# Kernel tuning notes

Measured on AMD Instinct MI355X. Metric: run time of the kernel, lower is better.

## Reference

```python
import jax, jax.numpy as jnp
import numpy as np

N_NODES = 20000
N_EDGES = 640000
IN_FEATS = 128
H1, H2 = 64, 32


def setup_inputs() -> dict:
    key = jax.random.key(0)
    ks = jax.random.split(key, 7)
    features = jax.random.normal(ks[0], (N_NODES, IN_FEATS), dtype=jnp.float32)
    W1 = jax.random.normal(ks[1], (IN_FEATS, H1), dtype=jnp.float32) * (1.0 / np.sqrt(IN_FEATS))
    b1 = jax.random.normal(ks[2], (H1,), dtype=jnp.float32) * 0.01
    W2 = jax.random.normal(ks[3], (H1, H2), dtype=jnp.float32) * (1.0 / np.sqrt(H1))
    b2 = jax.random.normal(ks[4], (H2,), dtype=jnp.float32) * 0.01
    src = jax.random.randint(ks[5], (N_EDGES,), 0, N_NODES, dtype=jnp.int32)
    dst = jax.random.randint(ks[6], (N_EDGES,), 0, N_NODES, dtype=jnp.int32)
    return {"features": features, "W1": W1, "b1": b1, "W2": W2, "b2": b2,
            "src": src, "dst": dst}


def _gcn_aggregate(h, src, dst, n_nodes):
    # copy_u + sum: gather source-node features along edges, sum at destinations
    return jax.ops.segment_sum(h[src], dst, num_segments=n_nodes)


def reference(features, W1, b1, W2, b2, src, dst):
    n = features.shape[0]
    # layer 1: aggregate then linear, relu
    h = _gcn_aggregate(features, src, dst, n)          # [N, in_feats]
    x = jax.nn.relu(h @ W1 + b1)                       # [N, 64]
    # layer 2: aggregate then linear
    h2 = _gcn_aggregate(x, src, dst, n)                # [N, 64]
    return h2 @ W2 + b2                                # [N, 32]
```

## Files before the change

### kernel.cpp

```cpp
#include <hip/hip_runtime.h>


#define NF 128
#define H1 64
#define H2 32
#define CAP 128
#define CAPSH 7
#define NG8 8
#define SCHUNK 1024
#define FILL_BPG 80

__device__ __forceinline__ float blo(unsigned u){ return __uint_as_float(u << 16); }
__device__ __forceinline__ float bhi(unsigned u){ return __uint_as_float(u & 0xffff0000u); }
__device__ __forceinline__ unsigned short f2b(float f){
    unsigned x = __float_as_uint(f);
    return (unsigned short)((x + 0x7fffu + ((x >> 16) & 1u)) >> 16);
}

__launch_bounds__(256)
__global__ void k1_kernel(const float* __restrict__ F, const float* __restrict__ W1,
                          const int* __restrict__ src, const int* __restrict__ dst,
                          unsigned* __restrict__ staged, int* __restrict__ bofs,
                          unsigned short* __restrict__ P1b, int* __restrict__ cnt,
                          unsigned inv_sz, int n_nodes, int n_edges, int nsb) {
    __shared__ __align__(16) float w[NF * H1];
    __shared__ int lcnt[NG8 + 1];
    const int t = threadIdx.x;
    const int bid = blockIdx.x;

    if (bid < nsb) {
        unsigned* sorted = (unsigned*)w;
        int e0 = bid * SCHUNK;
        int ce = min(n_edges - e0, SCHUNK);
        if (t < NG8 + 1) lcnt[t] = 0;
        __syncthreads();
        int i4 = e0 + t * 4;
        int dd[4], ss[4], bb[4], pp[4];
        if (i4 + 4 <= n_edges) {
            int4 d4 = *(const int4*)(dst + i4);
            int4 s4 = *(const int4*)(src + i4);
            dd[0]=d4.x; dd[1]=d4.y; dd[2]=d4.z; dd[3]=d4.w;
            ss[0]=s4.x; ss[1]=s4.y; ss[2]=s4.z; ss[3]=s4.w;
        } else {
#pragma unroll
            for (int k = 0; k < 4; ++k) {
                int e = i4 + k;
                dd[k] = (e < n_edges) ? dst[e] : -1;
                ss[k] = (e < n_edges) ? src[e] : 0;
            }
        }
#pragma unroll
        for (int k = 0; k < 4; ++k) {
            if (dd[k] >= 0) {
                bb[k] = (int)(unsigned)(((unsigned long long)(unsigned)dd[k] * inv_sz) >> 32);
                pp[k] = atomicAdd(&lcnt[bb[k]], 1);
            }
        }
        __syncthreads();
        if (t == 0) {
            int run = 0;
#pragma unroll
            for (int i = 0; i < NG8 + 1; ++i) { int c = lcnt[i]; lcnt[i] = run; run += c; }
        }
        __syncthreads();
#pragma unroll
        for (int k = 0; k < 4; ++k)
            if (dd[k] >= 0)
                sorted[lcnt[bb[k]] + pp[k]] = ((unsigned)dd[k] << 16) | (unsigned)ss[k];
        __syncthreads();
        for (int j = t; j < ce; j += 256) staged[(size_t)bid * SCHUNK + j] = sorted[j];
        if (t < NG8 + 1) bofs[t * nsb + bid] = lcnt[t];
        return;
    }

    int gb = bid - nsb;
    int zi = gb * 256 + t;
    if (zi < n_nodes) cnt[zi] = 0;
    {
        const float4* w4 = (const float4*)W1;
        float4* ws4 = (float4*)w;
#pragma unroll
        for (int j = 0; j < 8; ++j) ws4[t + 256 * j] = w4[t + 256 * j];
    }
    __syncthreads();
    int wid = t >> 6, lane = t & 63;
    int row0 = gb * 32 + wid * 8;
#pragma unroll
    for (int r = 0; r < 8; ++r) {
        int row = row0 + r;
        if (row >= n_nodes) break;
        const float4* f4 = (const float4*)(F + (size_t)row * NF);
        float acc = 0.f;
#pragma unroll 8
        for (int k4 = 0; k4 < NF / 4; ++k4) {
            float4 fv = f4[k4];
            acc += fv.x * w[(k4 * 4 + 0) * H1 + lane];
            acc += fv.y * w[(k4 * 4 + 1) * H1 + lane];
            acc += fv.z * w[(k4 * 4 + 2) * H1 + lane];
            acc += fv.w * w[(k4 * 4 + 3) * H1 + lane];
        }
        P1b[(size_t)row * H1 + lane] = f2b(acc);
    }
}

__launch_bounds__(256)
__global__ void fill2_kernel(const unsigned* __restrict__ staged, const int* __restrict__ bofs,
                             int* __restrict__ cnt, unsigned short* __restrict__ slots,
                             int nsb) {
    int g = blockIdx.x & (NG8 - 1), gi = blockIdx.x >> 3;
    for (int sb = gi; sb < nsb; sb += FILL_BPG) {
        int st = bofs[g * nsb + sb];
        int en = bofs[(g + 1) * nsb + sb];
        const unsigned* seg = staged + (size_t)sb * SCHUNK;
        for (int j = st + threadIdx.x; j < en; j += 256) {
            unsigned u = seg[j];
            int d = u >> 16;
            int p = atomicAdd(&cnt[d], 1);
            if (p < CAP) slots[(d << CAPSH) + p] = (unsigned short)(u & 0xffffu);
        }
    }
}

__launch_bounds__(256)
__global__ void agg1gemm2_kernel(const unsigned short* __restrict__ P1b,
                                 const int* __restrict__ cnt, const unsigned short* __restrict__ slots,
                                 const float* __restrict__ b1, const float* __restrict__ W2,
                                 unsigned short* __restrict__ P2b, int n_nodes, int sz) {
    __shared__ float w2s[H1 * H2];
    __shared__ float arow[4][H1];
    {
        const float4* w4 = (const float4*)W2;
        float4* ws4 = (float4*)w2s;
#pragma unroll
        for (int j = 0; j < 2; ++j) ws4[threadIdx.x + 256 * j] = w4[threadIdx.x + 256 * j];
    }
    __syncthreads();
    int wid = threadIdx.x >> 6, lane = threadIdx.x & 63;
    int g = blockIdx.x & (NG8 - 1), gi = blockIdx.x >> 3;
    int ni = gi * 4 + wid;
    if (ni >= sz) return;
    int node = g * sz + ni;
    if (node >= n_nodes) return;
    int deg = min(cnt[node], CAP);
    int base = node << CAPSH;
    int q = lane >> 4, c = lane & 15;
    const uint2* P1v = (const uint2*)P1b;
    float a0=0.f,a1=0.f,a2=0.f,a3=0.f, b0=0.f,b1v=0.f,b2v=0.f,b3=0.f;
    float c0=0.f,c1=0.f,c2=0.f,c3=0.f, d0=0.f,d1=0.f,d2=0.f,d3=0.f;
    int i = 0;
    for (; i + 16 <= deg; i += 16) {
        int sA = slots[base + i + q];
        int sB = slots[base + i + 4 + q];
        int sC = slots[base + i + 8 + q];
        int sD = slots[base + i + 12 + q];
        uint2 uA = P1v[(sA << 4) + c];
        uint2 uB = P1v[(sB << 4) + c];
        uint2 uC = P1v[(sC << 4) + c];
        uint2 uD = P1v[(sD << 4) + c];
        a0 += blo(uA.x); a1 += bhi(uA.x); a2 += blo(uA.y); a3 += bhi(uA.y);
        b0 += blo(uB.x); b1v += bhi(uB.x); b2v += blo(uB.y); b3 += bhi(uB.y);
        c0 += blo(uC.x); c1 += bhi(uC.x); c2 += blo(uC.y); c3 += bhi(uC.y);
        d0 += blo(uD.x); d1 += bhi(uD.x); d2 += blo(uD.y); d3 += bhi(uD.y);
    }
    for (; i + 4 <= deg; i += 4) {
        int sA = slots[base + i + q];
        uint2 uA = P1v[(sA << 4) + c];
        a0 += blo(uA.x); a1 += bhi(uA.x); a2 += blo(uA.y); a3 += bhi(uA.y);
    }
    if (q < deg - i) {
        int sA = slots[base + i + q];
        uint2 uA = P1v[(sA << 4) + c];
        a0 += blo(uA.x); a1 += bhi(uA.x); a2 += blo(uA.y); a3 += bhi(uA.y);
    }
    a0 += b0 + c0 + d0; a1 += b1v + c1 + d1; a2 += b2v + c2 + d2; a3 += b3 + c3 + d3;
    a0 += __shfl_xor(a0, 16, 64); a0 += __shfl_xor(a0, 32, 64);
    a1 += __shfl_xor(a1, 16, 64); a1 += __shfl_xor(a1, 32, 64);
    a2 += __shfl_xor(a2, 16, 64); a2 += __shfl_xor(a2, 32, 64);
    a3 += __shfl_xor(a3, 16, 64); a3 += __shfl_xor(a3, 32, 64);
    if (q == 0) {
        float4 bb = *(const float4*)(b1 + 4 * c);
        float4 v;
        v.x = fmaxf(a0 + bb.x, 0.f);
        v.y = fmaxf(a1 + bb.y, 0.f);
        v.z = fmaxf(a2 + bb.z, 0.f);
        v.w = fmaxf(a3 + bb.w, 0.f);
        *(float4*)&arow[wid][4 * c] = v;
    }
    int half = lane >> 5, c32 = lane & 31, kb = half * 32;
    float acc2 = 0.f;
#pragma unroll
    for (int k = 0; k < 32; ++k) acc2 += arow[wid][kb + k] * w2s[(kb + k) * H2 + c32];
    acc2 += __shfl_xor(acc2, 32, 64);
    if (lane < 32) P2b[(size_t)node * H2 + c32] = f2b(acc2);
}

__launch_bounds__(256)
__global__ void agg2_kernel(const unsigned short* __restrict__ P2b,
                            const int* __restrict__ cnt, const unsigned short* __restrict__ slots,
                            const float* __restrict__ b2, float* __restrict__ out,
                            int n_nodes, int sz) {
    int wid = threadIdx.x >> 6, lane = threadIdx.x & 63;
    int g = blockIdx.x & (NG8 - 1), gi = blockIdx.x >> 3;
    int ni = gi * 4 + wid;
    if (ni >= sz) return;
    int node = g * sz + ni;
    if (node >= n_nodes) return;
    int deg = min(cnt[node], CAP);
    int base = node << CAPSH;
    int o = lane >> 3, c = lane & 7;
    const uint2* P2v = (const uint2*)P2b;
    float a0=0.f,a1=0.f,a2=0.f,a3=0.f, b0=0.f,b1v=0.f,b2v=0.f,b3=0.f;
    float c0=0.f,c1=0.f,c2=0.f,c3=0.f, d0=0.f,d1=0.f,d2=0.f,d3=0.f;
    int i = 0;
    for (; i + 32 <= deg; i += 32) {
        int sA = slots[base + i + o];
        int sB = slots[base + i + 8 + o];
        int sC = slots[base + i + 16 + o];
        int sD = slots[base + i + 24 + o];
        uint2 uA = P2v[(sA << 3) + c];
        uint2 uB = P2v[(sB << 3) + c];
        uint2 uC = P2v[(sC << 3) + c];
        uint2 uD = P2v[(sD << 3) + c];
        a0 += blo(uA.x); a1 += bhi(uA.x); a2 += blo(uA.y); a3 += bhi(uA.y);
        b0 += blo(uB.x); b1v += bhi(uB.x); b2v += blo(uB.y); b3 += bhi(uB.y);
        c0 += blo(uC.x); c1 += bhi(uC.x); c2 += blo(uC.y); c3 += bhi(uC.y);
        d0 += blo(uD.x); d1 += bhi(uD.x); d2 += blo(uD.y); d3 += bhi(uD.y);
    }
    for (; i + 8 <= deg; i += 8) {
        int sA = slots[base + i + o];
        uint2 uA = P2v[(sA << 3) + c];
        a0 += blo(uA.x); a1 += bhi(uA.x); a2 += blo(uA.y); a3 += bhi(uA.y);
    }
    if (o < deg - i) {
        int sA = slots[base + i + o];
        uint2 uA = P2v[(sA << 3) + c];
        a0 += blo(uA.x); a1 += bhi(uA.x); a2 += blo(uA.y); a3 += bhi(uA.y);
    }
    a0 += b0 + c0 + d0; a1 += b1v + c1 + d1; a2 += b2v + c2 + d2; a3 += b3 + c3 + d3;
    a0 += __shfl_xor(a0, 8, 64); a0 += __shfl_xor(a0, 16, 64); a0 += __shfl_xor(a0, 32, 64);
    a1 += __shfl_xor(a1, 8, 64); a1 += __shfl_xor(a1, 16, 64); a1 += __shfl_xor(a1, 32, 64);
    a2 += __shfl_xor(a2, 8, 64); a2 += __shfl_xor(a2, 16, 64); a2 += __shfl_xor(a2, 32, 64);
    a3 += __shfl_xor(a3, 8, 64); a3 += __shfl_xor(a3, 16, 64); a3 += __shfl_xor(a3, 32, 64);
    if (o == 0) {
        float4 bb = *(const float4*)(b2 + 4 * c);
        float4 v;
        v.x = a0 + bb.x; v.y = a1 + bb.y; v.z = a2 + bb.z; v.w = a3 + bb.w;
        *(float4*)(out + (size_t)node * H2 + 4 * c) = v;
    }
}

extern "C" void kernel_launch(void* const* d_in, const int* in_sizes, int n_in,
                              void* d_out, int out_size, void* d_ws, size_t ws_size,
                              hipStream_t stream) {
    const float* F  = (const float*)d_in[0];
    const float* W1 = (const float*)d_in[1];
    const float* b1 = (const float*)d_in[2];
    const float* W2 = (const float*)d_in[3];
    const float* b2 = (const float*)d_in[4];
    const int* src  = (const int*)d_in[5];
    const int* dst  = (const int*)d_in[6];
    float* out = (float*)d_out;

    int n_nodes = in_sizes[0] / NF;
    int n_edges = in_sizes[5];
    int sz = (n_nodes + NG8 - 1) / NG8;
    unsigned inv_sz = (unsigned)(((1ULL << 32) + sz - 1) / (unsigned)sz);
    int nsb = (n_edges + SCHUNK - 1) / SCHUNK;

    unsigned short* P1b = (unsigned short*)d_ws;
    unsigned short* P2b = P1b + (size_t)n_nodes * H1;
    unsigned short* slots = P2b + (size_t)n_nodes * H2;
    int* cnt = (int*)(slots + ((size_t)n_nodes << CAPSH));
    unsigned* staged = (unsigned*)(cnt + n_nodes);
    int* bofs = (int*)(staged + (size_t)nsb * SCHUNK);

    int g1 = nsb + (n_nodes + 31) / 32;
    k1_kernel<<<g1, 256, 0, stream>>>(F, W1, src, dst, staged, bofs, P1b, cnt,
                                      inv_sz, n_nodes, n_edges, nsb);
    fill2_kernel<<<FILL_BPG * NG8, 256, 0, stream>>>(staged, bofs, cnt, slots, nsb);
    int bpg = (sz + 3) / 4;
    agg1gemm2_kernel<<<bpg * NG8, 256, 0, stream>>>(P1b, cnt, slots, b1, W2, P2b, n_nodes, sz);
    agg2_kernel<<<bpg * NG8, 256, 0, stream>>>(P2b, cnt, slots, b2, out, n_nodes, sz);
}
```

Baseline: 96.88 us.

## Replace LDS atomics with wave ballot ranking and hold W1 in registers

The edge bucketing pass now ranks edges within each wave using ballot and popcount, then combines per-wave counts in shared memory, replacing the shared-memory atomics. The projection pass stops staging the full 32KB W1 in LDS and instead loads 64-row slices of W1 into registers per lane. This shrinks the kernel's LDS footprint from about 32KB to about 4KB, aiming for higher occupancy and less LDS atomic contention. In exchange it adds register pressure (64 weight floats plus 8 accumulators per lane) and repeated global W1 reads per block.

```diff
diff --git a/kernel.cpp b/kernel.cpp
--- a/kernel.cpp
+++ b/kernel.cpp
@@ -23,19 +23,20 @@
                           unsigned* __restrict__ staged, int* __restrict__ bofs,
                           unsigned short* __restrict__ P1b, int* __restrict__ cnt,
                           unsigned inv_sz, int n_nodes, int n_edges, int nsb) {
-    __shared__ __align__(16) float w[NF * H1];
-    __shared__ int lcnt[NG8 + 1];
+    __shared__ unsigned sorted[SCHUNK];
+    __shared__ int wcnt[4][NG8];
+    __shared__ int wbase[4][NG8];
+    __shared__ int bb0[NG8 + 1];
     const int t = threadIdx.x;
     const int bid = blockIdx.x;
+    const int wid = t >> 6, lane = t & 63;
 
     if (bid < nsb) {
-        unsigned* sorted = (unsigned*)w;
         int e0 = bid * SCHUNK;
         int ce = min(n_edges - e0, SCHUNK);
-        if (t < NG8 + 1) lcnt[t] = 0;
-        __syncthreads();
         int i4 = e0 + t * 4;
         int dd[4], ss[4], bb[4], pp[4];
+        bool val[4];
         if (i4 + 4 <= n_edges) {
             int4 d4 = *(const int4*)(dst + i4);
             int4 s4 = *(const int4*)(src + i4);
@@ -49,57 +50,82 @@
                 ss[k] = (e < n_edges) ? src[e] : 0;
             }
         }
+        unsigned long long lt = (1ULL << lane) - 1ULL;
 #pragma unroll
         for (int k = 0; k < 4; ++k) {
-            if (dd[k] >= 0) {
-                bb[k] = (int)(unsigned)(((unsigned long long)(unsigned)dd[k] * inv_sz) >> 32);
-                pp[k] = atomicAdd(&lcnt[bb[k]], 1);
+            val[k] = dd[k] >= 0;
+            bb[k] = val[k]
+                ? (int)(unsigned)(((unsigned long long)(unsigned)dd[k] * inv_sz) >> 32)
+                : 0;
+        }
+#pragma unroll
+        for (int b = 0; b < NG8; ++b) {
+            int running = 0;
+#pragma unroll
+            for (int k = 0; k < 4; ++k) {
+                unsigned long long m = __ballot(val[k] && (bb[k] == b));
+                if (val[k] && (bb[k] == b)) pp[k] = running + (int)__popcll(m & lt);
+                running += (int)__popcll(m);
             }
+            if (lane == 0) wcnt[wid][b] = running;
+        }
+        __syncthreads();
+        if (t < NG8) {
+            int tot = 0;
+#pragma unroll
+            for (int w = 0; w < 4; ++w) { wbase[w][t] = tot; tot += wcnt[w][t]; }
+            bb0[t] = tot;
         }
         __syncthreads();
         if (t == 0) {
             int run = 0;
 #pragma unroll
-            for (int i = 0; i < NG8 + 1; ++i) { int c = lcnt[i]; lcnt[i] = run; run += c; }
+            for (int b = 0; b < NG8; ++b) { int c = bb0[b]; bb0[b] = run; run += c; }
+            bb0[NG8] = run;
         }
         __syncthreads();
 #pragma unroll
         for (int k = 0; k < 4; ++k)
-            if (dd[k] >= 0)
-                sorted[lcnt[bb[k]] + pp[k]] = ((unsigned)dd[k] << 16) | (unsigned)ss[k];
+            if (val[k])
+                sorted[bb0[bb[k]] + wbase[wid][bb[k]] + pp[k]] =
+                    ((unsigned)dd[k] << 16) | (unsigned)ss[k];
         __syncthreads();
         for (int j = t; j < ce; j += 256) staged[(size_t)bid * SCHUNK + j] = sorted[j];
-        if (t < NG8 + 1) bofs[t * nsb + bid] = lcnt[t];
+        if (t < NG8 + 1) bofs[t * nsb + bid] = bb0[t];
         return;
     }
 
     int gb = bid - nsb;
     int zi = gb * 256 + t;
     if (zi < n_nodes) cnt[zi] = 0;
-    {
-        const float4* w4 = (const float4*)W1;
-        float4* ws4 = (float4*)w;
-#pragma unroll
-        for (int j = 0; j < 8; ++j) ws4[t + 256 * j] = w4[t + 256 * j];
-    }
-    __syncthreads();
-    int wid = t >> 6, lane = t & 63;
     int row0 = gb * 32 + wid * 8;
+    float acc[8] = {0.f, 0.f, 0.f, 0.f, 0.f, 0.f, 0.f, 0.f};
+#pragma unroll 1
+    for (int cc = 0; cc < 2; ++cc) {
+        const int c0 = cc * 64;
+        float wreg[64];
+#pragma unroll
+        for (int k = 0; k < 64; ++k) wreg[k] = W1[(c0 + k) * H1 + lane];
+#pragma unroll
+        for (int r = 0; r < 8; ++r) {
+            int row = row0 + r;
+            if (row < n_nodes) {
+                const float4* f4 = (const float4*)(F + (size_t)row * NF + c0);
+#pragma unroll
+                for (int k4 = 0; k4 < 16; ++k4) {
+                    float4 fv = f4[k4];
+                    acc[r] += fv.x * wreg[k4 * 4 + 0];
+                    acc[r] += fv.y * wreg[k4 * 4 + 1];
+                    acc[r] += fv.z * wreg[k4 * 4 + 2];
+                    acc[r] += fv.w * wreg[k4 * 4 + 3];
+                }
+            }
+        }
+    }
 #pragma unroll
     for (int r = 0; r < 8; ++r) {
         int row = row0 + r;
-        if (row >= n_nodes) break;
-        const float4* f4 = (const float4*)(F + (size_t)row * NF);
-        float acc = 0.f;
-#pragma unroll 8
-        for (int k4 = 0; k4 < NF / 4; ++k4) {
-            float4 fv = f4[k4];
-            acc += fv.x * w[(k4 * 4 + 0) * H1 + lane];
-            acc += fv.y * w[(k4 * 4 + 1) * H1 + lane];
-            acc += fv.z * w[(k4 * 4 + 2) * H1 + lane];
-            acc += fv.w * w[(k4 * 4 + 3) * H1 + lane];
-        }
-        P1b[(size_t)row * H1 + lane] = f2b(acc);
+        if (row < n_nodes) P1b[(size_t)row * H1 + lane] = f2b(acc[r]);
     }
 }
 
```

Measured after the change: 90.43 us. 1.07x faster.
